# Performance work log

Measured on AMD Instinct MI355X. Metric: run time of the kernel, lower is better.

Reference implementation:

```python
import jax, jax.numpy as jnp
import numpy as np

N = 50000        # nodes
E = 200000       # interior edges
EB = 40000       # boundary edges
WID = 32         # hidden width
KER = 6          # edge feature dim
DEPTH = 4


def setup_inputs() -> dict:
    key = jax.random.key(0)
    ks = jax.random.split(key, 24)
    f32 = jnp.float32

    def nrm(k, sh, s):
        return jax.random.normal(k, sh, dtype=f32) * s

    inp = {
        "x": nrm(ks[0], (N, 1), 1.0),
        "edge_index": jax.random.randint(ks[1], (2, E), 0, N),
        "edge_attr": jax.random.uniform(ks[2], (E, KER), dtype=f32),
        "edge_index_boundary": jax.random.randint(ks[3], (2, EB), 0, N),
        "edge_attr_boundary": jax.random.uniform(ks[4], (EB, KER), dtype=f32),
        # fc1: in_width=1 -> width
        "fc1_w": nrm(ks[5], (1, WID), 0.3), "fc1_b": jnp.zeros((WID,), f32),
        # kernel MLP 1: [6 -> 8 -> 32 -> 32*32], ReLU between layers, none at end
        "k1_w1": nrm(ks[6], (KER, WID // 4), 0.3), "k1_b1": jnp.zeros((WID // 4,), f32),
        "k1_w2": nrm(ks[7], (WID // 4, WID), 0.2), "k1_b2": jnp.zeros((WID,), f32),
        "k1_w3": nrm(ks[8], (WID, WID * WID), 0.05), "k1_b3": jnp.zeros((WID * WID,), f32),
        # kernel MLP 2 (boundary)
        "k2_w1": nrm(ks[9], (KER, WID // 4), 0.3), "k2_b1": jnp.zeros((WID // 4,), f32),
        "k2_w2": nrm(ks[10], (WID // 4, WID), 0.2), "k2_b2": jnp.zeros((WID,), f32),
        "k2_w3": nrm(ks[11], (WID, WID * WID), 0.05), "k2_b3": jnp.zeros((WID * WID,), f32),
        # NNConv root weights + biases
        "root1": nrm(ks[12], (WID, WID), 0.15), "bias1": jnp.zeros((WID,), f32),
        "root2": nrm(ks[13], (WID, WID), 0.15), "bias2": jnp.zeros((WID,), f32),
        # fc2: width -> 1
        "fc2_w": nrm(ks[14], (WID, 1), 0.2), "fc2_b": jnp.zeros((1,), f32),
    }
    return inp


def _kernel_mlp(ea, w1, b1, w2, b2, w3, b3):
    # DenseNet: ReLU between layers, no final nonlinearity -> per-edge [W, W] matrices
    h = jax.nn.relu(ea @ w1 + b1)
    h = jax.nn.relu(h @ w2 + b2)
    return (h @ w3 + b3).reshape(-1, WID, WID)


def _nnconv(x, src, dst, We, root, bias):
    # message: gather x_j then per-edge matmul  [E, W] x [E, W, W] -> [E, W]
    msg = jnp.einsum('ei,eio->eo', x[src], We)
    agg = jax.ops.segment_sum(msg, dst, num_segments=N)
    cnt = jax.ops.segment_sum(jnp.ones((src.shape[0], 1), msg.dtype), dst, num_segments=N)
    mean = agg / jnp.maximum(cnt, 1.0)  # isolated nodes -> 0
    return mean + x @ root + bias


def reference(x, edge_index, edge_attr, edge_index_boundary, edge_attr_boundary,
              fc1_w, fc1_b,
              k1_w1, k1_b1, k1_w2, k1_b2, k1_w3, k1_b3,
              k2_w1, k2_b1, k2_w2, k2_b2, k2_w3, k2_b3,
              root1, bias1, root2, bias2,
              fc2_w, fc2_b):
    src, dst = edge_index[0], edge_index[1]
    srcb, dstb = edge_index_boundary[0], edge_index_boundary[1]
    # edge-conditioned weight matrices are x-independent: hoist out of depth loop
    W1 = _kernel_mlp(edge_attr, k1_w1, k1_b1, k1_w2, k1_b2, k1_w3, k1_b3)
    W2 = _kernel_mlp(edge_attr_boundary, k2_w1, k2_b1, k2_w2, k2_b2, k2_w3, k2_b3)

    h = x @ fc1_w + fc1_b  # [N, W]
    for _ in range(DEPTH):
        h = jax.nn.relu(_nnconv(h, src, dst, W1, root1, bias1)
                        + _nnconv(h, srcb, dstb, W2, root2, bias2))
    return h @ fc2_w + fc2_b  # [N, 1]
```

## Files before the change

kernel.cpp:

```cpp
#include <hip/hip_runtime.h>
#include <hip/hip_bf16.h>

#define WID 32
#define KER 6
#define DEPTH 4
#define WEXT_ELEMS (33 * 2 * 64 * 8)

typedef __attribute__((ext_vector_type(8))) short bf16x8;
typedef __attribute__((ext_vector_type(4))) float f32x4;

static __device__ __forceinline__ float bf2f(unsigned short u) {
  union { unsigned int u; float f; } v; v.u = ((unsigned int)u) << 16; return v.f;
}
static __device__ __forceinline__ unsigned short f2bf(float f) {
  union { float f; unsigned int u; } v; v.f = f;
  unsigned int r = v.u + 0x7fffu + ((v.u >> 16) & 1u);
  return (unsigned short)(r >> 16);
}

__global__ void k_pro(const int* __restrict__ ei, int E,
                      const int* __restrict__ eib, int EB,
                      unsigned int* __restrict__ cnt12, int n_nodes,
                      unsigned int* __restrict__ rank1, unsigned int* __restrict__ rank2,
                      const float* __restrict__ x, const float* __restrict__ fc1w,
                      const float* __restrict__ fc1b, float* __restrict__ h,
                      unsigned short* __restrict__ hbf,
                      const float* __restrict__ k1w3, const float* __restrict__ k1b3,
                      unsigned short* __restrict__ w1b,
                      const float* __restrict__ k2w3, const float* __restrict__ k2b3,
                      unsigned short* __restrict__ w2b,
                      int nbC, int nbH) {
  int bid = blockIdx.x, tid = threadIdx.x;
  if (bid < nbC) {
    int idx = bid * 256 + tid;
    if (idx < E) rank1[idx] = atomicAdd(&cnt12[ei[E + idx]], 1u);
    else if (idx < E + EB) { int e = idx - E; rank2[e] = atomicAdd(&cnt12[n_nodes + eib[EB + e]], 1u); }
  } else if (bid < nbC + nbH) {
    int gid = (bid - nbC) * 256 + tid;
    if (gid < n_nodes * WID) {
      int n = gid >> 5, o = gid & 31;
      float v = x[n] * fc1w[o] + fc1b[o];
      h[gid] = v; hbf[gid] = f2bf(v);
    }
  } else {
    int idx = (bid - nbC - nbH) * 256 + tid;
    if (idx < 2 * WEXT_ELEMS) {
      int which = idx >= WEXT_ELEMS;
      int id2 = which ? idx - WEXT_ELEMS : idx;
      const float* w3 = which ? k2w3 : k1w3;
      const float* b3 = which ? k2b3 : k1b3;
      unsigned short* outp = which ? w2b : w1b;
      int j = id2 & 7, l = (id2 >> 3) & 63, tt = (id2 >> 9) & 1, s = id2 >> 10;
      int p = ((l >> 4) << 3) + j;
      int o = tt * 16 + (l & 15);
      float v = (s < 32) ? w3[s * 1024 + p * 32 + o] : b3[p * 32 + o];
      outp[id2] = f2bf(v);
    }
  }
}

__global__ void k_scan1(const unsigned int* __restrict__ cnt, unsigned int* __restrict__ partials,
                        int n2) {
  __shared__ unsigned int s[256];
  int t = threadIdx.x;
  int i = blockIdx.x * 256 + t;
  unsigned int v = (i < n2) ? cnt[i] : 0u;
  s[t] = v;
  __syncthreads();
  for (int d = 128; d > 0; d >>= 1) {
    if (t < d) s[t] += s[t + d];
    __syncthreads();
  }
  if (t == 0) partials[blockIdx.x] = s[0];
}

__global__ void k_scan2(unsigned int* __restrict__ partials, int nb) {
  __shared__ unsigned int s[1024];
  int t = threadIdx.x;
  unsigned int v = (t < nb) ? partials[t] : 0u;
  s[t] = v;
  __syncthreads();
  for (int d = 1; d < 1024; d <<= 1) {
    unsigned int u = (t >= d) ? s[t - d] : 0u;
    __syncthreads();
    s[t] += u;
    __syncthreads();
  }
  if (t < nb) partials[t] = s[t] - v;
}

__global__ void k_scan3(const unsigned int* __restrict__ cnt, const unsigned int* __restrict__ partials,
                        unsigned int* __restrict__ start1, unsigned int* __restrict__ start2,
                        int n, int Etot) {
  __shared__ unsigned int s[256];
  int t = threadIdx.x;
  int i = blockIdx.x * 256 + t;
  int n2 = 2 * n;
  unsigned int v = (i < n2) ? cnt[i] : 0u;
  s[t] = v;
  __syncthreads();
  for (int d = 1; d < 256; d <<= 1) {
    unsigned int u = (t >= d) ? s[t - d] : 0u;
    __syncthreads();
    s[t] += u;
    __syncthreads();
  }
  unsigned int ex = s[t] - v + partials[blockIdx.x];
  if (i < n) start1[i] = ex;
  else if (i < n2) start2[i - n] = ex - (unsigned int)Etot;
}

__global__ void k_emlp2(const float* __restrict__ ea1, const int* __restrict__ ei, int E,
                        const unsigned int* __restrict__ rank1, const unsigned int* __restrict__ start1,
                        const float* __restrict__ k1w1, const float* __restrict__ k1b1,
                        const float* __restrict__ k1w2, const float* __restrict__ k1b2,
                        unsigned short* __restrict__ h3s1, int* __restrict__ ssrc1,
                        const float* __restrict__ ea2, const int* __restrict__ eib, int EB,
                        const unsigned int* __restrict__ rank2, const unsigned int* __restrict__ start2,
                        const float* __restrict__ k2w1, const float* __restrict__ k2b1,
                        const float* __restrict__ k2w2, const float* __restrict__ k2b2,
                        unsigned short* __restrict__ h3s2, int* __restrict__ ssrc2,
                        int nbE) {
  bool role1 = (int)blockIdx.x < nbE;
  const float* ea  = role1 ? ea1 : ea2;
  const int* eidx  = role1 ? ei : eib;
  int ecnt         = role1 ? E : EB;
  const unsigned int* rank  = role1 ? rank1 : rank2;
  const unsigned int* start = role1 ? start1 : start2;
  const float* w1 = role1 ? k1w1 : k2w1;
  const float* b1 = role1 ? k1b1 : k2b1;
  const float* w2 = role1 ? k1w2 : k2w2;
  const float* b2 = role1 ? k1b2 : k2b2;
  unsigned short* h3s = role1 ? h3s1 : h3s2;
  int* ssrc = role1 ? ssrc1 : ssrc2;
  int blk0 = role1 ? blockIdx.x : blockIdx.x - nbE;

  __shared__ float sw1[KER * 8], sb1[8], sw2[8 * WID], sb2[WID];
  int tid = threadIdx.x;
  if (tid < KER * 8) sw1[tid] = w1[tid];
  if (tid < 8) sb1[tid] = b1[tid];
  if (tid < 8 * WID) sw2[tid] = w2[tid];
  if (tid < WID) sb2[tid] = b2[tid];
  __syncthreads();
  int e = blk0 * 256 + tid;
  if (e >= ecnt) return;
  float a[KER];
  #pragma unroll
  for (int i = 0; i < KER; i++) a[i] = ea[e * KER + i];
  float h8[8];
  #pragma unroll
  for (int o = 0; o < 8; o++) {
    float s = sb1[o];
    #pragma unroll
    for (int i = 0; i < KER; i++) s += a[i] * sw1[i * 8 + o];
    h8[o] = fmaxf(s, 0.f);
  }
  int d = eidx[ecnt + e];
  unsigned int p = start[d] + rank[e];
  ssrc[p] = eidx[e];
  unsigned int words[16];
  #pragma unroll
  for (int m = 0; m < 16; m++) {
    float s0 = sb2[2 * m], s1 = sb2[2 * m + 1];
    #pragma unroll
    for (int i = 0; i < 8; i++) {
      s0 += h8[i] * sw2[i * WID + 2 * m];
      s1 += h8[i] * sw2[i * WID + 2 * m + 1];
    }
    words[m] = (unsigned int)f2bf(fmaxf(s0, 0.f)) | ((unsigned int)f2bf(fmaxf(s1, 0.f)) << 16);
  }
  uint4* dst = (uint4*)(h3s + (size_t)p * WID);
  dst[0] = make_uint4(words[0], words[1], words[2], words[3]);
  dst[1] = make_uint4(words[4], words[5], words[6], words[7]);
  dst[2] = make_uint4(words[8], words[9], words[10], words[11]);
  dst[3] = make_uint4(words[12], words[13], words[14], words[15]);
}

__launch_bounds__(512)
__global__ void k_msg2(const unsigned short* __restrict__ hbf,
                       const unsigned short* __restrict__ h3s1, const int* __restrict__ ssrc1,
                       int ecnt1, const unsigned short* __restrict__ w1,
                       unsigned short* __restrict__ msg1,
                       const unsigned short* __restrict__ h3s2, const int* __restrict__ ssrc2,
                       int ecnt2, const unsigned short* __restrict__ w2,
                       unsigned short* __restrict__ msg2, int B1) {
  const unsigned short* h3s; const int* ssrc; const unsigned short* wext;
  unsigned short* msgbuf; int ecnt, blk0, nblk;
  if ((int)blockIdx.x < B1) {
    h3s = h3s1; ssrc = ssrc1; wext = w1; msgbuf = msg1; ecnt = ecnt1;
    blk0 = blockIdx.x; nblk = B1;
  } else {
    h3s = h3s2; ssrc = ssrc2; wext = w2; msgbuf = msg2; ecnt = ecnt2;
    blk0 = blockIdx.x - B1; nblk = gridDim.x - B1;
  }
  __shared__ __align__(16) unsigned short wlds[WEXT_ELEMS];
  {
    const uint4* s4 = (const uint4*)wext;
    uint4* d4 = (uint4*)wlds;
    for (int i = threadIdx.x; i < WEXT_ELEMS / 8; i += blockDim.x) d4[i] = s4[i];
  }
  __syncthreads();
  const int lane = threadIdx.x & 63;
  const int wv = threadIdx.x >> 6;
  const int g = lane >> 4, eo = lane & 15;
  const int ntile = (ecnt + 15) >> 4;
  const int wpb = blockDim.x >> 6;
  const int nwv = nblk * wpb;
  for (int tile = blk0 * wpb + wv; tile < ntile; tile += nwv) {
    const int e = min((tile << 4) + eo, ecnt - 1);
    const int srcn = ssrc[e];
    const uint4* h3p = (const uint4*)(h3s + (size_t)e * WID);
    uint4 q0 = h3p[0], q1 = h3p[1], q2 = h3p[2], q3 = h3p[3];
    unsigned int h3w[16];
    h3w[0]=q0.x; h3w[1]=q0.y; h3w[2]=q0.z; h3w[3]=q0.w;
    h3w[4]=q1.x; h3w[5]=q1.y; h3w[6]=q1.z; h3w[7]=q1.w;
    h3w[8]=q2.x; h3w[9]=q2.y; h3w[10]=q2.z; h3w[11]=q2.w;
    h3w[12]=q3.x; h3w[13]=q3.y; h3w[14]=q3.z; h3w[15]=q3.w;
    uint4 hq = *(const uint4*)(hbf + (size_t)srcn * WID + g * 8);
    bf16x8 hsv = __builtin_bit_cast(bf16x8, hq);
    float hsf[8];
    #pragma unroll
    for (int j = 0; j < 8; j++) hsf[j] = bf2f((unsigned short)hsv[j]);
    f32x4 acc0 = {0.f, 0.f, 0.f, 0.f};
    f32x4 acc1 = {0.f, 0.f, 0.f, 0.f};
    #pragma unroll
    for (int s = 0; s < 32; s++) {
      unsigned int wrd = h3w[s >> 1];
      unsigned int fb = (s & 1) ? (wrd & 0xffff0000u) : (wrd << 16);
      float h3f = __builtin_bit_cast(float, fb);
      float p0 = h3f * hsf[0], p1 = h3f * hsf[1], p2 = h3f * hsf[2], p3 = h3f * hsf[3];
      float p4 = h3f * hsf[4], p5 = h3f * hsf[5], p6 = h3f * hsf[6], p7 = h3f * hsf[7];
      uint4 aw;
      asm("v_cvt_pk_bf16_f32 %0, %1, %2" : "=v"(aw.x) : "v"(p0), "v"(p1));
      asm("v_cvt_pk_bf16_f32 %0, %1, %2" : "=v"(aw.y) : "v"(p2), "v"(p3));
      asm("v_cvt_pk_bf16_f32 %0, %1, %2" : "=v"(aw.z) : "v"(p4), "v"(p5));
      asm("v_cvt_pk_bf16_f32 %0, %1, %2" : "=v"(aw.w) : "v"(p6), "v"(p7));
      bf16x8 af = __builtin_bit_cast(bf16x8, aw);
      bf16x8 b0 = *(const bf16x8*)&wlds[((s * 2 + 0) * 64 + lane) * 8];
      bf16x8 b1 = *(const bf16x8*)&wlds[((s * 2 + 1) * 64 + lane) * 8];
      acc0 = __builtin_amdgcn_mfma_f32_16x16x32_bf16(af, b0, acc0, 0, 0, 0);
      acc1 = __builtin_amdgcn_mfma_f32_16x16x32_bf16(af, b1, acc1, 0, 0, 0);
    }
    {
      bf16x8 b0 = *(const bf16x8*)&wlds[((32 * 2 + 0) * 64 + lane) * 8];
      bf16x8 b1 = *(const bf16x8*)&wlds[((32 * 2 + 1) * 64 + lane) * 8];
      acc0 = __builtin_amdgcn_mfma_f32_16x16x32_bf16(hsv, b0, acc0, 0, 0, 0);
      acc1 = __builtin_amdgcn_mfma_f32_16x16x32_bf16(hsv, b1, acc1, 0, 0, 0);
    }
    #pragma unroll
    for (int r = 0; r < 4; r++) {
      int oe = (tile << 4) + g * 4 + r;
      if (oe < ecnt) {
        msgbuf[(size_t)oe * WID + eo]      = f2bf(acc0[r]);
        msgbuf[(size_t)oe * WID + 16 + eo] = f2bf(acc1[r]);
      }
    }
  }
}

__global__ void k_update(const unsigned short* __restrict__ msg1,
                         const unsigned short* __restrict__ msg2,
                         const unsigned int* __restrict__ start1, const unsigned int* __restrict__ cnt1,
                         const unsigned int* __restrict__ start2, const unsigned int* __restrict__ cnt2,
                         const float* __restrict__ root1, const float* __restrict__ root2,
                         const float* __restrict__ bias1, const float* __restrict__ bias2,
                         float* __restrict__ h, unsigned short* __restrict__ hbf,
                         int last, const float* __restrict__ fc2w, const float* __restrict__ fc2b,
                         float* __restrict__ out, int n_nodes) {
  __shared__ float rs[WID * WID];
  __shared__ float bs[WID];
  __shared__ float hrow[8][WID];
  int tid = threadIdx.x;
  for (int i = tid; i < WID * WID; i += blockDim.x) rs[i] = root1[i] + root2[i];
  if (tid < WID) bs[tid] = bias1[tid] + bias2[tid];
  int o = tid & 31, nl = tid >> 5;
  int n = blockIdx.x * 8 + nl;
  bool ok = (n < n_nodes);
  hrow[nl][o] = ok ? h[(size_t)n * WID + o] : 0.f;
  __syncthreads();
  if (!ok) return;
  unsigned int b1 = start1[n], c1 = cnt1[n];
  unsigned int b2 = start2[n], c2 = cnt2[n];
  float s1 = 0.f, s2 = 0.f;
  for (unsigned int k = 0; k < c1; k++) s1 += bf2f(msg1[(size_t)(b1 + k) * WID + o]);
  for (unsigned int k = 0; k < c2; k++) s2 += bf2f(msg2[(size_t)(b2 + k) * WID + o]);
  float v = s1 / (float)(c1 ? c1 : 1u) + s2 / (float)(c2 ? c2 : 1u) + bs[o];
  #pragma unroll
  for (int i = 0; i < WID; i++) v += hrow[nl][i] * rs[i * WID + o];
  v = fmaxf(v, 0.f);
  h[(size_t)n * WID + o] = v;
  hbf[(size_t)n * WID + o] = f2bf(v);
  if (last) {
    float pv = v * fc2w[o];
    #pragma unroll
    for (int m = 16; m >= 1; m >>= 1) pv += __shfl_xor(pv, m, 32);
    if (o == 0) out[n] = pv + fc2b[0];
  }
}

extern "C" void kernel_launch(void* const* d_in, const int* in_sizes, int n_in,
                              void* d_out, int out_size, void* d_ws, size_t ws_size,
                              hipStream_t stream) {
  const float* x    = (const float*)d_in[0];
  const int*   ei   = (const int*)d_in[1];
  const float* ea   = (const float*)d_in[2];
  const int*   eib  = (const int*)d_in[3];
  const float* eab  = (const float*)d_in[4];
  const float* fc1w = (const float*)d_in[5];
  const float* fc1b = (const float*)d_in[6];
  const float* k1w1 = (const float*)d_in[7];
  const float* k1b1 = (const float*)d_in[8];
  const float* k1w2 = (const float*)d_in[9];
  const float* k1b2 = (const float*)d_in[10];
  const float* k1w3 = (const float*)d_in[11];
  const float* k1b3 = (const float*)d_in[12];
  const float* k2w1 = (const float*)d_in[13];
  const float* k2b1 = (const float*)d_in[14];
  const float* k2w2 = (const float*)d_in[15];
  const float* k2b2 = (const float*)d_in[16];
  const float* k2w3 = (const float*)d_in[17];
  const float* k2b3 = (const float*)d_in[18];
  const float* root1 = (const float*)d_in[19];
  const float* bias1 = (const float*)d_in[20];
  const float* root2 = (const float*)d_in[21];
  const float* bias2 = (const float*)d_in[22];
  const float* fc2w = (const float*)d_in[23];
  const float* fc2b = (const float*)d_in[24];
  float* out = (float*)d_out;

  const int n_nodes = in_sizes[0];
  const int E  = in_sizes[1] / 2;
  const int EB = in_sizes[3] / 2;

  char* ws = (char*)d_ws;
  size_t off = 0;
  auto alloc = [&](size_t bytes) -> void* {
    void* p = ws + off;
    off = (off + bytes + 255) & ~(size_t)255;
    return p;
  };
  unsigned short* h3s1 = (unsigned short*)alloc((size_t)E * WID * 2);
  unsigned short* h3s2 = (unsigned short*)alloc((size_t)EB * WID * 2);
  unsigned short* w1b  = (unsigned short*)alloc((size_t)WEXT_ELEMS * 2);
  unsigned short* w2b  = (unsigned short*)alloc((size_t)WEXT_ELEMS * 2);
  float* h             = (float*)alloc((size_t)n_nodes * WID * 4);
  unsigned short* hbf  = (unsigned short*)alloc((size_t)n_nodes * WID * 2);
  unsigned short* msg1 = (unsigned short*)alloc((size_t)E * WID * 2);
  unsigned short* msg2 = (unsigned short*)alloc((size_t)EB * WID * 2);
  unsigned int* cnt12  = (unsigned int*)alloc((size_t)2 * n_nodes * 4);
  unsigned int* cnt1 = cnt12;
  unsigned int* cnt2 = cnt12 + n_nodes;
  unsigned int* start1 = (unsigned int*)alloc((size_t)n_nodes * 4);
  unsigned int* start2 = (unsigned int*)alloc((size_t)n_nodes * 4);
  unsigned int* rank1  = (unsigned int*)alloc((size_t)E * 4);
  unsigned int* rank2  = (unsigned int*)alloc((size_t)EB * 4);
  int* ssrc1 = (int*)alloc((size_t)E * 4);
  int* ssrc2 = (int*)alloc((size_t)EB * 4);
  unsigned int* partials = (unsigned int*)alloc((size_t)1024 * 4);
  (void)ws_size; (void)n_in; (void)out_size;

  const int n2 = 2 * n_nodes;
  const int nb = (n2 + 255) / 256;
  const int nbC = (E + EB + 255) / 256;
  const int nbH = (n_nodes * WID + 255) / 256;
  const int nbP = (2 * WEXT_ELEMS + 255) / 256;
  const int nbE = (E + 255) / 256;
  const int nbEB = (EB + 255) / 256;

  hipMemsetAsync(cnt12, 0, (size_t)n2 * 4, stream);
  k_pro<<<nbC + nbH + nbP, 256, 0, stream>>>(ei, E, eib, EB, cnt12, n_nodes, rank1, rank2,
                                             x, fc1w, fc1b, h, hbf,
                                             k1w3, k1b3, w1b, k2w3, k2b3, w2b, nbC, nbH);
  k_scan1<<<nb, 256, 0, stream>>>(cnt12, partials, n2);
  k_scan2<<<1, 1024, 0, stream>>>(partials, nb);
  k_scan3<<<nb, 256, 0, stream>>>(cnt12, partials, start1, start2, n_nodes, E);
  k_emlp2<<<nbE + nbEB, 256, 0, stream>>>(ea, ei, E, rank1, start1, k1w1, k1b1, k1w2, k1b2, h3s1, ssrc1,
                                          eab, eib, EB, rank2, start2, k2w1, k2b1, k2w2, k2b2, h3s2, ssrc2,
                                          nbE);

  const int GRID = 512;
  int B1 = (int)(((long long)GRID * E) / (E + EB));
  if (B1 < 1) B1 = 1;
  if (B1 > GRID - 1) B1 = GRID - 1;

  for (int t = 0; t < DEPTH; t++) {
    k_msg2<<<GRID, 512, 0, stream>>>(hbf, h3s1, ssrc1, E, w1b, msg1,
                                     h3s2, ssrc2, EB, w2b, msg2, B1);
    int last = (t == DEPTH - 1);
    k_update<<<(n_nodes + 7) / 8, 256, 0, stream>>>(msg1, msg2, start1, cnt1, start2, cnt2,
                                                    root1, root2, bias1, bias2, h, hbf,
                                                    last, fc2w, fc2b, out, n_nodes);
  }
}
```

Measured before the change: 325.9 us.

## Switch message MFMA to 32x32x16 tiles and vectorize node update

The per-edge message kernel now processes 32 edges per wavefront using the 32x32x16 bf16 MFMA with a single 16-register accumulator instead of two 16x16x32 accumulators, and the prepacked weight layout is reorganized to match. The node update kernel now handles 64 nodes per block with 4 threads per node, using 16-byte vector loads of messages and h and vector stores. The aim is fewer MFMA issues and LDS reads per edge, plus wider, less scattered memory traffic in the update. In exchange, the per-thread A-operand build work doubles and the message store pattern changes to scalar column writes.

```diff
diff --git a/kernel.cpp b/kernel.cpp
--- a/kernel.cpp
+++ b/kernel.cpp
@@ -4,10 +4,11 @@
 #define WID 32
 #define KER 6
 #define DEPTH 4
-#define WEXT_ELEMS (33 * 2 * 64 * 8)
+#define W32_ELEMS (66 * 64 * 8)
 
 typedef __attribute__((ext_vector_type(8))) short bf16x8;
 typedef __attribute__((ext_vector_type(4))) float f32x4;
+typedef __attribute__((ext_vector_type(16))) float f32x16;
 
 static __device__ __forceinline__ float bf2f(unsigned short u) {
   union { unsigned int u; float f; } v; v.u = ((unsigned int)u) << 16; return v.f;
@@ -44,16 +45,24 @@
     }
   } else {
     int idx = (bid - nbC - nbH) * 256 + tid;
-    if (idx < 2 * WEXT_ELEMS) {
-      int which = idx >= WEXT_ELEMS;
-      int id2 = which ? idx - WEXT_ELEMS : idx;
+    if (idx < 2 * W32_ELEMS) {
+      int which = idx >= W32_ELEMS;
+      int id2 = which ? idx - W32_ELEMS : idx;
       const float* w3 = which ? k2w3 : k1w3;
       const float* b3 = which ? k2b3 : k1b3;
       unsigned short* outp = which ? w2b : w1b;
-      int j = id2 & 7, l = (id2 >> 3) & 63, tt = (id2 >> 9) & 1, s = id2 >> 10;
-      int p = ((l >> 4) << 3) + j;
-      int o = tt * 16 + (l & 15);
-      float v = (s < 32) ? w3[s * 1024 + p * 32 + o] : b3[p * 32 + o];
+      int j = id2 & 7, l = (id2 >> 3) & 63, s = id2 >> 9;
+      int o = l & 31;
+      float v;
+      if (s < 64) {
+        int m = s >> 1;
+        int i = ((s & 1) << 4) + ((l >> 5) << 3) + j;
+        v = w3[m * 1024 + i * 32 + o];
+      } else {
+        int t2 = s - 64;
+        int i = (t2 << 4) + ((l >> 5) << 3) + j;
+        v = b3[i * 32 + o];
+      }
       outp[id2] = f2bf(v);
     }
   }
@@ -177,13 +186,13 @@
 }
 
 __launch_bounds__(512)
-__global__ void k_msg2(const unsigned short* __restrict__ hbf,
-                       const unsigned short* __restrict__ h3s1, const int* __restrict__ ssrc1,
-                       int ecnt1, const unsigned short* __restrict__ w1,
-                       unsigned short* __restrict__ msg1,
-                       const unsigned short* __restrict__ h3s2, const int* __restrict__ ssrc2,
-                       int ecnt2, const unsigned short* __restrict__ w2,
-                       unsigned short* __restrict__ msg2, int B1) {
+__global__ void k_msg32(const unsigned short* __restrict__ hbf,
+                        const unsigned short* __restrict__ h3s1, const int* __restrict__ ssrc1,
+                        int ecnt1, const unsigned short* __restrict__ w1,
+                        unsigned short* __restrict__ msg1,
+                        const unsigned short* __restrict__ h3s2, const int* __restrict__ ssrc2,
+                        int ecnt2, const unsigned short* __restrict__ w2,
+                        unsigned short* __restrict__ msg2, int B1) {
   const unsigned short* h3s; const int* ssrc; const unsigned short* wext;
   unsigned short* msgbuf; int ecnt, blk0, nblk;
   if ((int)blockIdx.x < B1) {
@@ -193,21 +202,22 @@
     h3s = h3s2; ssrc = ssrc2; wext = w2; msgbuf = msg2; ecnt = ecnt2;
     blk0 = blockIdx.x - B1; nblk = gridDim.x - B1;
   }
-  __shared__ __align__(16) unsigned short wlds[WEXT_ELEMS];
+  __shared__ __align__(16) unsigned short wlds[W32_ELEMS];
   {
     const uint4* s4 = (const uint4*)wext;
     uint4* d4 = (uint4*)wlds;
-    for (int i = threadIdx.x; i < WEXT_ELEMS / 8; i += blockDim.x) d4[i] = s4[i];
+    for (int i = threadIdx.x; i < W32_ELEMS / 8; i += blockDim.x) d4[i] = s4[i];
   }
   __syncthreads();
   const int lane = threadIdx.x & 63;
-  const int wv = threadIdx.x >> 6;
-  const int g = lane >> 4, eo = lane & 15;
-  const int ntile = (ecnt + 15) >> 4;
+  const int wvid = threadIdx.x >> 6;
+  const int col = lane & 31, kg = lane >> 5;
+  const int base = kg << 3;
+  const int ntile = (ecnt + 31) >> 5;
   const int wpb = blockDim.x >> 6;
   const int nwv = nblk * wpb;
-  for (int tile = blk0 * wpb + wv; tile < ntile; tile += nwv) {
-    const int e = min((tile << 4) + eo, ecnt - 1);
+  for (int tile = blk0 * wpb + wvid; tile < ntile; tile += nwv) {
+    const int e = min((tile << 5) + col, ecnt - 1);
     const int srcn = ssrc[e];
     const uint4* h3p = (const uint4*)(h3s + (size_t)e * WID);
     uint4 q0 = h3p[0], q1 = h3p[1], q2 = h3p[2], q3 = h3p[3];
@@ -216,44 +226,51 @@
     h3w[4]=q1.x; h3w[5]=q1.y; h3w[6]=q1.z; h3w[7]=q1.w;
     h3w[8]=q2.x; h3w[9]=q2.y; h3w[10]=q2.z; h3w[11]=q2.w;
     h3w[12]=q3.x; h3w[13]=q3.y; h3w[14]=q3.z; h3w[15]=q3.w;
-    uint4 hq = *(const uint4*)(hbf + (size_t)srcn * WID + g * 8);
-    bf16x8 hsv = __builtin_bit_cast(bf16x8, hq);
-    float hsf[8];
-    #pragma unroll
-    for (int j = 0; j < 8; j++) hsf[j] = bf2f((unsigned short)hsv[j]);
-    f32x4 acc0 = {0.f, 0.f, 0.f, 0.f};
-    f32x4 acc1 = {0.f, 0.f, 0.f, 0.f};
-    #pragma unroll
-    for (int s = 0; s < 32; s++) {
-      unsigned int wrd = h3w[s >> 1];
-      unsigned int fb = (s & 1) ? (wrd & 0xffff0000u) : (wrd << 16);
+    uint4 hqA = *(const uint4*)(hbf + (size_t)srcn * WID + base);
+    uint4 hqB = *(const uint4*)(hbf + (size_t)srcn * WID + 16 + base);
+    bf16x8 hsvA = __builtin_bit_cast(bf16x8, hqA);
+    bf16x8 hsvB = __builtin_bit_cast(bf16x8, hqB);
+    float hfA[8], hfB[8];
+    #pragma unroll
+    for (int j = 0; j < 8; j++) { hfA[j] = bf2f((unsigned short)hsvA[j]); hfB[j] = bf2f((unsigned short)hsvB[j]); }
+    f32x16 acc = {0.f,0.f,0.f,0.f,0.f,0.f,0.f,0.f,0.f,0.f,0.f,0.f,0.f,0.f,0.f,0.f};
+    #pragma unroll
+    for (int sp = 0; sp < 32; sp++) {
+      unsigned int wrd = h3w[sp >> 1];
+      unsigned int fb = (sp & 1) ? (wrd & 0xffff0000u) : (wrd << 16);
       float h3f = __builtin_bit_cast(float, fb);
-      float p0 = h3f * hsf[0], p1 = h3f * hsf[1], p2 = h3f * hsf[2], p3 = h3f * hsf[3];
-      float p4 = h3f * hsf[4], p5 = h3f * hsf[5], p6 = h3f * hsf[6], p7 = h3f * hsf[7];
+      float p0 = h3f*hfA[0], p1 = h3f*hfA[1], p2 = h3f*hfA[2], p3 = h3f*hfA[3];
+      float p4 = h3f*hfA[4], p5 = h3f*hfA[5], p6 = h3f*hfA[6], p7 = h3f*hfA[7];
       uint4 aw;
       asm("v_cvt_pk_bf16_f32 %0, %1, %2" : "=v"(aw.x) : "v"(p0), "v"(p1));
       asm("v_cvt_pk_bf16_f32 %0, %1, %2" : "=v"(aw.y) : "v"(p2), "v"(p3));
       asm("v_cvt_pk_bf16_f32 %0, %1, %2" : "=v"(aw.z) : "v"(p4), "v"(p5));
       asm("v_cvt_pk_bf16_f32 %0, %1, %2" : "=v"(aw.w) : "v"(p6), "v"(p7));
       bf16x8 af = __builtin_bit_cast(bf16x8, aw);
-      bf16x8 b0 = *(const bf16x8*)&wlds[((s * 2 + 0) * 64 + lane) * 8];
-      bf16x8 b1 = *(const bf16x8*)&wlds[((s * 2 + 1) * 64 + lane) * 8];
-      acc0 = __builtin_amdgcn_mfma_f32_16x16x32_bf16(af, b0, acc0, 0, 0, 0);
-      acc1 = __builtin_amdgcn_mfma_f32_16x16x32_bf16(af, b1, acc1, 0, 0, 0);
+      bf16x8 b0 = *(const bf16x8*)&wlds[(((sp * 2 + 0) * 64) + lane) * 8];
+      acc = __builtin_amdgcn_mfma_f32_32x32x16_bf16(af, b0, acc, 0, 0, 0);
+      float q0f = h3f*hfB[0], q1f = h3f*hfB[1], q2f = h3f*hfB[2], q3f = h3f*hfB[3];
+      float q4f = h3f*hfB[4], q5f = h3f*hfB[5], q6f = h3f*hfB[6], q7f = h3f*hfB[7];
+      uint4 aw2;
+      asm("v_cvt_pk_bf16_f32 %0, %1, %2" : "=v"(aw2.x) : "v"(q0f), "v"(q1f));
+      asm("v_cvt_pk_bf16_f32 %0, %1, %2" : "=v"(aw2.y) : "v"(q2f), "v"(q3f));
+      asm("v_cvt_pk_bf16_f32 %0, %1, %2" : "=v"(aw2.z) : "v"(q4f), "v"(q5f));
+      asm("v_cvt_pk_bf16_f32 %0, %1, %2" : "=v"(aw2.w) : "v"(q6f), "v"(q7f));
+      bf16x8 af2 = __builtin_bit_cast(bf16x8, aw2);
+      bf16x8 b1 = *(const bf16x8*)&wlds[(((sp * 2 + 1) * 64) + lane) * 8];
+      acc = __builtin_amdgcn_mfma_f32_32x32x16_bf16(af2, b1, acc, 0, 0, 0);
     }
     {
-      bf16x8 b0 = *(const bf16x8*)&wlds[((32 * 2 + 0) * 64 + lane) * 8];
-      bf16x8 b1 = *(const bf16x8*)&wlds[((32 * 2 + 1) * 64 + lane) * 8];
-      acc0 = __builtin_amdgcn_mfma_f32_16x16x32_bf16(hsv, b0, acc0, 0, 0, 0);
-      acc1 = __builtin_amdgcn_mfma_f32_16x16x32_bf16(hsv, b1, acc1, 0, 0, 0);
-    }
-    #pragma unroll
-    for (int r = 0; r < 4; r++) {
-      int oe = (tile << 4) + g * 4 + r;
-      if (oe < ecnt) {
-        msgbuf[(size_t)oe * WID + eo]      = f2bf(acc0[r]);
-        msgbuf[(size_t)oe * WID + 16 + eo] = f2bf(acc1[r]);
-      }
+      bf16x8 b64 = *(const bf16x8*)&wlds[((64 * 64) + lane) * 8];
+      bf16x8 b65 = *(const bf16x8*)&wlds[((65 * 64) + lane) * 8];
+      acc = __builtin_amdgcn_mfma_f32_32x32x16_bf16(hsvA, b64, acc, 0, 0, 0);
+      acc = __builtin_amdgcn_mfma_f32_32x32x16_bf16(hsvB, b65, acc, 0, 0, 0);
+    }
+    #pragma unroll
+    for (int r = 0; r < 16; r++) {
+      int row = (r & 3) + 8 * (r >> 2) + 4 * kg;
+      int oe = (tile << 5) + row;
+      if (oe < ecnt) msgbuf[(size_t)oe * WID + col] = f2bf(acc[r]);
     }
   }
 }
@@ -269,32 +286,64 @@
                          float* __restrict__ out, int n_nodes) {
   __shared__ float rs[WID * WID];
   __shared__ float bs[WID];
-  __shared__ float hrow[8][WID];
+  __shared__ float hsh[64][WID + 1];
   int tid = threadIdx.x;
-  for (int i = tid; i < WID * WID; i += blockDim.x) rs[i] = root1[i] + root2[i];
+  for (int i = tid; i < WID * WID; i += 256) rs[i] = root1[i] + root2[i];
   if (tid < WID) bs[tid] = bias1[tid] + bias2[tid];
-  int o = tid & 31, nl = tid >> 5;
-  int n = blockIdx.x * 8 + nl;
+  int nl = tid >> 2, qc = (tid & 3) << 3;
+  int n = blockIdx.x * 64 + nl;
   bool ok = (n < n_nodes);
-  hrow[nl][o] = ok ? h[(size_t)n * WID + o] : 0.f;
+  if (ok) {
+    float4 va = *(const float4*)(h + (size_t)n * WID + qc);
+    float4 vb = *(const float4*)(h + (size_t)n * WID + qc + 4);
+    hsh[nl][qc+0]=va.x; hsh[nl][qc+1]=va.y; hsh[nl][qc+2]=va.z; hsh[nl][qc+3]=va.w;
+    hsh[nl][qc+4]=vb.x; hsh[nl][qc+5]=vb.y; hsh[nl][qc+6]=vb.z; hsh[nl][qc+7]=vb.w;
+  }
   __syncthreads();
   if (!ok) return;
   unsigned int b1 = start1[n], c1 = cnt1[n];
   unsigned int b2 = start2[n], c2 = cnt2[n];
-  float s1 = 0.f, s2 = 0.f;
-  for (unsigned int k = 0; k < c1; k++) s1 += bf2f(msg1[(size_t)(b1 + k) * WID + o]);
-  for (unsigned int k = 0; k < c2; k++) s2 += bf2f(msg2[(size_t)(b2 + k) * WID + o]);
-  float v = s1 / (float)(c1 ? c1 : 1u) + s2 / (float)(c2 ? c2 : 1u) + bs[o];
-  #pragma unroll
-  for (int i = 0; i < WID; i++) v += hrow[nl][i] * rs[i * WID + o];
-  v = fmaxf(v, 0.f);
-  h[(size_t)n * WID + o] = v;
-  hbf[(size_t)n * WID + o] = f2bf(v);
+  float s1[8] = {0,0,0,0,0,0,0,0}, s2[8] = {0,0,0,0,0,0,0,0};
+  for (unsigned int k = 0; k < c1; k++) {
+    uint4 mw = *(const uint4*)(msg1 + (size_t)(b1 + k) * WID + qc);
+    s1[0] += bf2f((unsigned short)(mw.x & 0xffffu)); s1[1] += bf2f((unsigned short)(mw.x >> 16));
+    s1[2] += bf2f((unsigned short)(mw.y & 0xffffu)); s1[3] += bf2f((unsigned short)(mw.y >> 16));
+    s1[4] += bf2f((unsigned short)(mw.z & 0xffffu)); s1[5] += bf2f((unsigned short)(mw.z >> 16));
+    s1[6] += bf2f((unsigned short)(mw.w & 0xffffu)); s1[7] += bf2f((unsigned short)(mw.w >> 16));
+  }
+  for (unsigned int k = 0; k < c2; k++) {
+    uint4 mw = *(const uint4*)(msg2 + (size_t)(b2 + k) * WID + qc);
+    s2[0] += bf2f((unsigned short)(mw.x & 0xffffu)); s2[1] += bf2f((unsigned short)(mw.x >> 16));
+    s2[2] += bf2f((unsigned short)(mw.y & 0xffffu)); s2[3] += bf2f((unsigned short)(mw.y >> 16));
+    s2[4] += bf2f((unsigned short)(mw.z & 0xffffu)); s2[5] += bf2f((unsigned short)(mw.z >> 16));
+    s2[6] += bf2f((unsigned short)(mw.w & 0xffffu)); s2[7] += bf2f((unsigned short)(mw.w >> 16));
+  }
+  float c1f = (float)(c1 ? c1 : 1u), c2f = (float)(c2 ? c2 : 1u);
+  float v[8];
+  #pragma unroll
+  for (int j = 0; j < 8; j++) v[j] = s1[j] / c1f + s2[j] / c2f + bs[qc + j];
+  #pragma unroll
+  for (int i = 0; i < WID; i++) {
+    float hv = hsh[nl][i];
+    #pragma unroll
+    for (int j = 0; j < 8; j++) v[j] += hv * rs[i * WID + qc + j];
+  }
+  #pragma unroll
+  for (int j = 0; j < 8; j++) v[j] = fmaxf(v[j], 0.f);
+  *(float4*)(h + (size_t)n * WID + qc)     = make_float4(v[0], v[1], v[2], v[3]);
+  *(float4*)(h + (size_t)n * WID + qc + 4) = make_float4(v[4], v[5], v[6], v[7]);
+  unsigned int pw0 = (unsigned int)f2bf(v[0]) | ((unsigned int)f2bf(v[1]) << 16);
+  unsigned int pw1 = (unsigned int)f2bf(v[2]) | ((unsigned int)f2bf(v[3]) << 16);
+  unsigned int pw2 = (unsigned int)f2bf(v[4]) | ((unsigned int)f2bf(v[5]) << 16);
+  unsigned int pw3 = (unsigned int)f2bf(v[6]) | ((unsigned int)f2bf(v[7]) << 16);
+  *(uint4*)(hbf + (size_t)n * WID + qc) = make_uint4(pw0, pw1, pw2, pw3);
   if (last) {
-    float pv = v * fc2w[o];
-    #pragma unroll
-    for (int m = 16; m >= 1; m >>= 1) pv += __shfl_xor(pv, m, 32);
-    if (o == 0) out[n] = pv + fc2b[0];
+    float pv = 0.f;
+    #pragma unroll
+    for (int j = 0; j < 8; j++) pv += v[j] * fc2w[qc + j];
+    pv += __shfl_xor(pv, 1, 4);
+    pv += __shfl_xor(pv, 2, 4);
+    if ((tid & 3) == 0) out[n] = pv + fc2b[0];
   }
 }
 
@@ -341,8 +390,8 @@
   };
   unsigned short* h3s1 = (unsigned short*)alloc((size_t)E * WID * 2);
   unsigned short* h3s2 = (unsigned short*)alloc((size_t)EB * WID * 2);
-  unsigned short* w1b  = (unsigned short*)alloc((size_t)WEXT_ELEMS * 2);
-  unsigned short* w2b  = (unsigned short*)alloc((size_t)WEXT_ELEMS * 2);
+  unsigned short* w1b  = (unsigned short*)alloc((size_t)W32_ELEMS * 2);
+  unsigned short* w2b  = (unsigned short*)alloc((size_t)W32_ELEMS * 2);
   float* h             = (float*)alloc((size_t)n_nodes * WID * 4);
   unsigned short* hbf  = (unsigned short*)alloc((size_t)n_nodes * WID * 2);
   unsigned short* msg1 = (unsigned short*)alloc((size_t)E * WID * 2);
@@ -363,7 +412,7 @@
   const int nb = (n2 + 255) / 256;
   const int nbC = (E + EB + 255) / 256;
   const int nbH = (n_nodes * WID + 255) / 256;
-  const int nbP = (2 * WEXT_ELEMS + 255) / 256;
+  const int nbP = (2 * W32_ELEMS + 255) / 256;
   const int nbE = (E + 255) / 256;
   const int nbEB = (EB + 255) / 256;
 
@@ -384,11 +433,11 @@
   if (B1 > GRID - 1) B1 = GRID - 1;
 
   for (int t = 0; t < DEPTH; t++) {
-    k_msg2<<<GRID, 512, 0, stream>>>(hbf, h3s1, ssrc1, E, w1b, msg1,
-                                     h3s2, ssrc2, EB, w2b, msg2, B1);
+    k_msg32<<<GRID, 512, 0, stream>>>(hbf, h3s1, ssrc1, E, w1b, msg1,
+                                      h3s2, ssrc2, EB, w2b, msg2, B1);
     int last = (t == DEPTH - 1);
-    k_update<<<(n_nodes + 7) / 8, 256, 0, stream>>>(msg1, msg2, start1, cnt1, start2, cnt2,
-                                                    root1, root2, bias1, bias2, h, hbf,
-                                                    last, fc2w, fc2b, out, n_nodes);
-  }
-}
+    k_update<<<(n_nodes + 63) / 64, 256, 0, stream>>>(msg1, msg2, start1, cnt1, start2, cnt2,
+                                                      root1, root2, bias1, bias2, h, hbf,
+                                                      last, fc2w, fc2b, out, n_nodes);
+  }
+}
```

After: 297.1 us. 1.1x faster.
